# Performance work log

Hardware: AMD Instinct MI355X
Metric: run time of the kernel (lower is better)

The kernel has to match this reference:

```python
import jax, jax.numpy as jnp
import numpy as np

RADIUS_VIEWPOOL = 0.075  # self.view_pool_radius
EPS_BN = 1e-5


def _pconv(x, w, b):
    # 1x1 Conv1d: x (B, Cin, N), w (Cout, Cin), b (Cout,)
    return jnp.einsum('oc,bcn->bon', w, x) + b[None, :, None]


def _bn(x, p):
    # eval-mode BatchNorm1d; p rows: gamma, beta, running_mean, running_var
    g, b, m, v = p[0], p[1], p[2], p[3]
    inv = g * jax.lax.rsqrt(v + EPS_BN)
    return (x - m[None, :, None]) * inv[None, :, None] + b[None, :, None]


def setup_inputs() -> dict:
    key = jax.random.key(0)
    it = iter(jax.random.split(key, 80))
    Np, Nr = 16384, 8192
    inp = {}
    inp['pcd_xyz'] = jax.random.uniform(next(it), (1, Np, 3), jnp.float32)
    inp['rgb_xyz'] = jax.random.uniform(next(it), (1, Nr, 3), jnp.float32)
    inp['pcd_features'] = jax.random.normal(next(it), (1, 32, Np), jnp.float32)
    inp['rgb_features'] = jax.random.normal(next(it), (1, 128, Nr), jnp.float32)

    def conv(name, o, c):
        s = 1.0 / np.sqrt(c)
        inp[name + '_w'] = jax.random.uniform(next(it), (o, c), jnp.float32, -s, s)
        inp[name + '_b'] = jax.random.uniform(next(it), (o,), jnp.float32, -s, s)

    def bn(name, c):
        g = 1.0 + 0.1 * jax.random.normal(next(it), (c,), jnp.float32)
        b = 0.1 * jax.random.normal(next(it), (c,), jnp.float32)
        m = 0.1 * jax.random.normal(next(it), (c,), jnp.float32)
        v = jax.random.uniform(next(it), (c,), jnp.float32, 0.5, 1.5)
        inp[name] = jnp.stack([g, b, m, v])

    conv('cc1', 384, 384); bn('cc_bn', 384); conv('cc2', 128, 384)
    conv('co1', 256, 256); bn('co_bn', 256); conv('co2', 128, 256)
    conv('dh1', 160, 160); bn('dh1_bn', 160)
    conv('dh2', 160, 160); bn('dh2_bn', 160)
    conv('dh3', 128, 160)
    conv('sh1', 128, 128); bn('sh_bn', 128)
    conv('sh2', 1, 128)
    return inp


def _forward(pcd_xyz, rgb_xyz, pcd_features, rgb_features,
             cc1_w, cc1_b, cc_bn, cc2_w, cc2_b,
             co1_w, co1_b, co_bn, co2_w, co2_b,
             dh1_w, dh1_b, dh1_bn, dh2_w, dh2_b, dh2_bn, dh3_w, dh3_b,
             sh1_w, sh1_b, sh_bn, sh2_w, sh2_b):
    Np = pcd_xyz.shape[1]
    Nr = rgb_xyz.shape[1]
    C_rgb = rgb_features.shape[1]

    # ---- three_nn: 3 nearest rgb points for each pcd point ----
    d2 = jnp.sum((pcd_xyz[0, :, None, :] - rgb_xyz[0, None, :, :]) ** 2, axis=-1)  # (Np, Nr)
    neg_d2, idx = jax.lax.top_k(-d2, 3)                     # (Np, 3)
    dist = jnp.sqrt(jnp.maximum(-neg_d2, 0.0))
    # idx[dist > radius] = -1 in torch -> indexes shadow (zero) row appended at end
    neighbor = jnp.where(dist > RADIUS_VIEWPOOL, Nr, idx)   # (Np, 3)

    rgb_f = jnp.concatenate([rgb_features[0].T,
                             jnp.zeros((1, C_rgb), rgb_features.dtype)], axis=0)  # (Nr+1, 128)
    nf = rgb_f[neighbor]                                    # (Np, 3, 128) gather
    max_features = nf.max(axis=1)                           # (Np, 128)

    # fuception fusion: conv over concatenated neighbor features, then fuse with max
    x_cat = nf.reshape(Np, 3 * C_rgb).T[None]               # (1, 384, Np)
    h = jax.nn.relu(_bn(_pconv(x_cat, cc1_w, cc1_b), cc_bn))
    concat_out = _pconv(h, cc2_w, cc2_b)                    # (1, 128, Np)
    x2 = jnp.concatenate([concat_out, max_features.T[None]], axis=1)  # (1, 256, Np)
    h = jax.nn.relu(_bn(_pconv(x2, co1_w, co1_b), co_bn))
    attach = _pconv(h, co2_w, co2_b)                        # (1, 128, Np)

    # fuse pcd + assigned rgb features -> direct feature header (160 = 128+32)
    full = jnp.concatenate([pcd_features, attach], axis=1)  # (1, 160, Np)
    h = jax.nn.relu(_bn(_pconv(full, dh1_w, dh1_b), dh1_bn))
    h = jax.nn.relu(_bn(_pconv(h, dh2_w, dh2_b), dh2_bn))
    fp = _pconv(h, dh3_w, dh3_b)                            # (1, 128, Np)

    # score header: conv-bn-relu-conv-sigmoid
    s = jax.nn.relu(_bn(_pconv(fp, sh1_w, sh1_b), sh_bn))
    vote_scores = jax.nn.sigmoid(_pconv(s, sh2_w, sh2_b))[0, 0]  # (Np,)

    # L2-normalized vote features (N, 128)
    vf = fp[0].T
    vf = vf / jnp.maximum(jnp.linalg.norm(vf, axis=1, keepdims=True), 1e-12)
    return pcd_xyz[0], vote_scores, vf


def reference(pcd_xyz, rgb_xyz, pcd_features, rgb_features,
              cc1_w, cc1_b, cc_bn, cc2_w, cc2_b,
              co1_w, co1_b, co_bn, co2_w, co2_b,
              dh1_w, dh1_b, dh1_bn, dh2_w, dh2_b, dh2_bn, dh3_w, dh3_b,
              sh1_w, sh1_b, sh_bn, sh2_w, sh2_b):
    return _forward(pcd_xyz, rgb_xyz, pcd_features, rgb_features,
                    cc1_w, cc1_b, cc_bn, cc2_w, cc2_b,
                    co1_w, co1_b, co_bn, co2_w, co2_b,
                    dh1_w, dh1_b, dh1_bn, dh2_w, dh2_b, dh2_bn, dh3_w, dh3_b,
                    sh1_w, sh1_b, sh_bn, sh2_w, sh2_b)
```

## Files before the change

kernel.cpp:

```cpp
#include <hip/hip_runtime.h>
#include <math.h>

#define NP 16384
#define NR 8192
#define GRID 13
#define NCELL (GRID * GRID * GRID)
#define CAP 28

typedef __attribute__((ext_vector_type(8))) short short8;
typedef __attribute__((ext_vector_type(4))) float f32x4;

__device__ inline unsigned short f2b(float f) {
  unsigned int x = __float_as_uint(f);
  return (unsigned short)((x + 0x7FFFu + ((x >> 16) & 1u)) >> 16);
}
__device__ inline float blo(unsigned int u) { return __uint_as_float(u << 16); }
__device__ inline float bhi(unsigned int u) { return __uint_as_float(u & 0xffff0000u); }

__global__ __launch_bounds__(256) void k_pre(const float* __restrict__ rf,
                                             const float* __restrict__ rxyz,
                                             const float* __restrict__ pf,
                                             const float* __restrict__ s0, const float* __restrict__ s1,
                                             const float* __restrict__ s2, const float* __restrict__ s3,
                                             const float* __restrict__ s4, const float* __restrict__ s5,
                                             const float* __restrict__ s6, const float* __restrict__ s7,
                                             unsigned short* __restrict__ rgbTb,
                                             float4* __restrict__ rxyz4,
                                             unsigned short* __restrict__ fullp,
                                             unsigned short* __restrict__ dst,
                                             int* __restrict__ cellCnt) {
  __shared__ float tile[128][65];
  int b = blockIdx.x, t = threadIdx.x;
  if (b < 128) {
    int r0 = b * 64;
    for (int e = 0; e < 32; ++e) {
      int idx = t + e * 256;
      int c = idx >> 6, rl = idx & 63;
      tile[c][rl] = rf[c * NR + r0 + rl];
    }
    __syncthreads();
    for (int e = 0; e < 32; ++e) {
      int idx = t + e * 256;
      int rl = idx >> 7, c = idx & 127;
      rgbTb[(size_t)(r0 + rl) * 128 + c] = f2b(tile[c][rl]);
    }
    if (b == 0 && t < 128) rgbTb[(size_t)NR * 128 + t] = 0;
    if ((t >> 6) == 0) {
      int i = r0 + (t & 63);
      float x = rxyz[i * 3], y = rxyz[i * 3 + 1], z = rxyz[i * 3 + 2];
      rxyz4[i] = make_float4(x, y, z, 0.f);
    }
  } else if (b < 384) {
    int n0 = (b - 128) * 64;
    for (int e = 0; e < 8; ++e) {
      int idx = t + e * 256;
      int c = idx >> 6, nl = idx & 63;
      tile[c][nl] = pf[c * NP + n0 + nl];
    }
    __syncthreads();
    for (int e = 0; e < 8; ++e) {
      int idx = t + e * 256;
      int nl = idx >> 5, c = idx & 31;
      fullp[(size_t)(n0 + nl) * 32 + c] = f2b(tile[c][nl]);
    }
  } else if (b < 960) {
    const int groups[8] = {18432, 6144, 8192, 4096, 3200, 3200, 2560, 2048};
    const int Cs[8]     = {384, 384, 256, 256, 160, 160, 160, 128};
    const int offs[8]   = {0, 147456, 196608, 262144, 294912, 320512, 346112, 366592};
    const float* srcs[8] = {s0, s1, s2, s3, s4, s5, s6, s7};
    int j = b - 384;
    int m = j / 72, bx = j % 72;
    int gidx = bx * 256 + t;
    if (gidx >= groups[m]) return;
    int C = Cs[m], NC = C >> 5;
    int ot = gidx / (NC * 64);
    int rem = gidx - ot * (NC * 64);
    int k = rem >> 6, lane = rem & 63;
    int q = lane >> 4, l15 = lane & 15;
    const float* sp = srcs[m] + (size_t)(ot * 16 + l15) * C + k * 32 + q * 8;
    float4 a = *(const float4*)sp, c4 = *(const float4*)(sp + 4);
    uint4 o;
    o.x = f2b(a.x) | ((unsigned int)f2b(a.y) << 16);
    o.y = f2b(a.z) | ((unsigned int)f2b(a.w) << 16);
    o.z = f2b(c4.x) | ((unsigned int)f2b(c4.y) << 16);
    o.w = f2b(c4.z) | ((unsigned int)f2b(c4.w) << 16);
    *(uint4*)(dst + offs[m] + (size_t)gidx * 8) = o;
  } else {
    int idx = (b - 960) * 256 + t;
    if (idx < NCELL) cellCnt[idx] = 0;
  }
}

__global__ __launch_bounds__(64) void k_build(const float4* __restrict__ rxyz4,
                                              int* __restrict__ cellCnt,
                                              float4* __restrict__ cellTab) {
  int i = blockIdx.x * 64 + threadIdx.x;
  float4 r = rxyz4[i];
  int cx = (int)(r.x * 13.f); cx = cx < 0 ? 0 : (cx > 12 ? 12 : cx);
  int cy = (int)(r.y * 13.f); cy = cy < 0 ? 0 : (cy > 12 ? 12 : cy);
  int cz = (int)(r.z * 13.f); cz = cz < 0 ? 0 : (cz > 12 ? 12 : cz);
  int cell = (cz * 13 + cy) * 13 + cx;
  int slot = atomicAdd(&cellCnt[cell], 1);
  if (slot < CAP) cellTab[(size_t)cell * CAP + slot] = make_float4(r.x, r.y, r.z, __int_as_float(i));
}

template <int C, int O, int COFF, bool BN, bool RELU>
__device__ __forceinline__ void mlp_layer(const unsigned short* __restrict__ W,
                                          const float* __restrict__ bias,
                                          const float* __restrict__ bnp,
                                          const unsigned short* Xs,
                                          unsigned short* Ys,
                                          int wo, int q, int l15, int lane) {
  constexpr int NC = C / 32;
  constexpr int NT = O / 16;
  constexpr int MT = (NT + 7) / 8;
  f32x4 acc[MT][2];
  short8 afb[2][MT];
  const unsigned short* wp[MT];
#pragma unroll
  for (int i = 0; i < MT; ++i) {
    acc[i][0] = (f32x4){0.f, 0.f, 0.f, 0.f};
    acc[i][1] = (f32x4){0.f, 0.f, 0.f, 0.f};
    int ot = wo + i * 8;
    wp[i] = W + ((size_t)(((ot < NT) ? ot : 0) * NC) * 64 + lane) * 8;
  }
#pragma unroll
  for (int k = 0; k < 2 && k < NC; ++k)
#pragma unroll
    for (int i = 0; i < MT; ++i)
      if (wo + i * 8 < NT) afb[k][i] = *(const short8*)(wp[i] + (size_t)k * 512);
  short8 bf0 = *(const short8*)&Xs[l15 * 392 + q * 8];
  short8 bf1 = *(const short8*)&Xs[(16 + l15) * 392 + q * 8];
#pragma unroll
  for (int k = 0; k < NC; ++k) {
    short8 nbf0 = bf0, nbf1 = bf1;
    if (k + 1 < NC) {
      nbf0 = *(const short8*)&Xs[l15 * 392 + (k + 1) * 32 + q * 8];
      nbf1 = *(const short8*)&Xs[(16 + l15) * 392 + (k + 1) * 32 + q * 8];
    }
    int slot = k & 1;
#pragma unroll
    for (int i = 0; i < MT; ++i) {
      if (wo + i * 8 < NT) {
        acc[i][0] = __builtin_amdgcn_mfma_f32_16x16x32_bf16(afb[slot][i], bf0, acc[i][0], 0, 0, 0);
        acc[i][1] = __builtin_amdgcn_mfma_f32_16x16x32_bf16(afb[slot][i], bf1, acc[i][1], 0, 0, 0);
      }
    }
    if (k + 2 < NC) {
#pragma unroll
      for (int i = 0; i < MT; ++i)
        if (wo + i * 8 < NT) afb[slot][i] = *(const short8*)(wp[i] + (size_t)(k + 2) * 512);
    }
    bf0 = nbf0; bf1 = nbf1;
  }
#pragma unroll
  for (int i = 0; i < MT; ++i) {
    int ot = wo + i * 8;
    if (ot >= NT) continue;
    int o4 = ot * 16 + q * 4;
    f32x4 bb = *(const f32x4*)(bias + o4);
    f32x4 sc, sh;
    if (BN) {
      f32x4 g  = *(const f32x4*)(bnp + o4);
      f32x4 be = *(const f32x4*)(bnp + O + o4);
      f32x4 mm = *(const f32x4*)(bnp + 2 * O + o4);
      f32x4 vv = *(const f32x4*)(bnp + 3 * O + o4);
#pragma unroll
      for (int r = 0; r < 4; ++r) {
        float inv = g[r] * rsqrtf(vv[r] + 1e-5f);
        sc[r] = inv; sh[r] = (bb[r] - mm[r]) * inv + be[r];
      }
    } else {
      sc = (f32x4){1.f, 1.f, 1.f, 1.f}; sh = bb;
    }
#pragma unroll
    for (int rt = 0; rt < 2; ++rt) {
      ushort4 u;
#pragma unroll
      for (int r = 0; r < 4; ++r) {
        float x = acc[i][rt][r] * sc[r] + sh[r];
        if (RELU) x = fmaxf(x, 0.f);
        ((unsigned short*)&u)[r] = f2b(x);
      }
      *(ushort4*)&Ys[(rt * 16 + l15) * 392 + COFF + ot * 16 + q * 4] = u;
    }
  }
}

__global__ __launch_bounds__(512) void k_mlp(
    const unsigned short* __restrict__ rgbTb,
    const float* __restrict__ pxyz,
    const int* __restrict__ cellCnt,
    const float4* __restrict__ cellTab,
    const unsigned short* __restrict__ fullp,
    const unsigned short* __restrict__ wcc1, const unsigned short* __restrict__ wcc2,
    const unsigned short* __restrict__ wco1, const unsigned short* __restrict__ wco2,
    const unsigned short* __restrict__ wdh1, const unsigned short* __restrict__ wdh2,
    const unsigned short* __restrict__ wdh3, const unsigned short* __restrict__ wsh1,
    const float* __restrict__ cc1_b, const float* __restrict__ cc_bn,
    const float* __restrict__ cc2_b,
    const float* __restrict__ co1_b, const float* __restrict__ co_bn,
    const float* __restrict__ co2_b,
    const float* __restrict__ dh1_b, const float* __restrict__ dh1_bn,
    const float* __restrict__ dh2_b, const float* __restrict__ dh2_bn,
    const float* __restrict__ dh3_b,
    const float* __restrict__ sh1_b, const float* __restrict__ sh_bn,
    const float* __restrict__ sh2_w, const float* __restrict__ sh2_b,
    float* __restrict__ out) {
  __shared__ unsigned short Ab[32 * 392];
  __shared__ unsigned short Bb[32 * 392];
  __shared__ int nbrS[32][3];
  int t = threadIdx.x, lane = t & 63, w = t >> 6;
  int wo = w & 7;
  int q = lane >> 4, l15 = lane & 15;
  int n0 = blockIdx.x * 32;
  {
    int n = n0 + w * 4 + q;
    float px = pxyz[n * 3], py = pxyz[n * 3 + 1], pz = pxyz[n * 3 + 2];
    int cx = (int)(px * 13.f); cx = cx < 0 ? 0 : (cx > 12 ? 12 : cx);
    int cy = (int)(py * 13.f); cy = cy < 0 ? 0 : (cy > 12 ? 12 : cy);
    int cz = (int)(pz * 13.f); cz = cz < 0 ? 0 : (cz > 12 ? 12 : cz);
    const float R2L = 0.005626125f;
    const unsigned long long SENT = ((unsigned long long)__float_as_uint(R2L) << 32);
    unsigned long long k0 = SENT, k1 = SENT, k2 = SENT;
    for (int ci = l15; ci < 27; ci += 16) {
      int dz = ci / 9 - 1, dyc = (ci / 3) % 3 - 1, dxc = ci % 3 - 1;
      int zz = cz + dz, yy = cy + dyc, xx = cx + dxc;
      if ((unsigned)zz <= 12u && (unsigned)yy <= 12u && (unsigned)xx <= 12u) {
        int c = (zz * 13 + yy) * 13 + xx;
        int m = cellCnt[c]; m = m < CAP ? m : CAP;
        const float4* tp = cellTab + (size_t)c * CAP;
        for (int k = 0; k < m; ++k) {
          float4 qq = tp[k];
          float dxx = qq.x - px, dyy = qq.y - py, dzz = qq.z - pz;
          float d2 = fmaf(dxx, dxx, fmaf(dyy, dyy, dzz * dzz));
          unsigned long long key =
              ((unsigned long long)__float_as_uint(d2) << 32) | (unsigned int)__float_as_int(qq.w);
          if (key < k2) {
            if (key < k1) {
              k2 = k1;
              if (key < k0) { k1 = k0; k0 = key; }
              else          { k1 = key; }
            } else k2 = key;
          }
        }
      }
    }
    int pos = 0;
    unsigned long long res[3];
#pragma unroll
    for (int r = 0; r < 3; ++r) {
      unsigned long long cur = (pos == 0) ? k0 : (pos == 1) ? k1 : (pos == 2) ? k2 : ~0ull;
      unsigned long long m = cur;
#pragma unroll
      for (int o = 1; o <= 8; o <<= 1) {
        unsigned long long other = __shfl_xor(m, o);
        m = other < m ? other : m;
      }
      res[r] = m;
      if (cur == m) ++pos;
    }
    if (l15 == 0) {
      const float R2 = 0.075f * 0.075f;
      float d0 = __uint_as_float((unsigned int)(res[0] >> 32));
      float d1 = __uint_as_float((unsigned int)(res[1] >> 32));
      float d2v = __uint_as_float((unsigned int)(res[2] >> 32));
      nbrS[w * 4 + q][0] = (d0 > R2) ? NR : (int)(res[0] & 0xffffffffu);
      nbrS[w * 4 + q][1] = (d1 > R2) ? NR : (int)(res[1] & 0xffffffffu);
      nbrS[w * 4 + q][2] = (d2v > R2) ? NR : (int)(res[2] & 0xffffffffu);
    }
  }
  __syncthreads();
  unsigned int mreg[4];
#pragma unroll
  for (int pj = 0; pj < 4; ++pj) {
    int r = w * 4 + pj;
    unsigned int j0 = (unsigned int)nbrS[r][0]; j0 = j0 > NR ? NR : j0;
    unsigned int j1 = (unsigned int)nbrS[r][1]; j1 = j1 > NR ? NR : j1;
    unsigned int j2 = (unsigned int)nbrS[r][2]; j2 = j2 > NR ? NR : j2;
    unsigned int a = ((const unsigned int*)(rgbTb + (size_t)j0 * 128))[lane];
    unsigned int b = ((const unsigned int*)(rgbTb + (size_t)j1 * 128))[lane];
    unsigned int c = ((const unsigned int*)(rgbTb + (size_t)j2 * 128))[lane];
    unsigned int* xr = (unsigned int*)&Ab[r * 392];
    xr[lane] = a; xr[64 + lane] = b; xr[128 + lane] = c;
    float ml = fmaxf(blo(a), fmaxf(blo(b), blo(c)));
    float mh = fmaxf(bhi(a), fmaxf(bhi(b), bhi(c)));
    mreg[pj] = (__float_as_uint(mh) & 0xffff0000u) | (__float_as_uint(ml) >> 16);
  }
  __syncthreads();
  mlp_layer<384, 384, 0, true,  true >(wcc1, cc1_b, cc_bn, Ab, Bb, wo, q, l15, lane);
  __syncthreads();
#pragma unroll
  for (int pj = 0; pj < 4; ++pj)
    ((unsigned int*)&Ab[(w * 4 + pj) * 392])[64 + lane] = mreg[pj];
  mlp_layer<384, 128, 0, false, false>(wcc2, cc2_b, nullptr, Bb, Ab, wo, q, l15, lane);
  __syncthreads();
  mlp_layer<256, 256, 0, true,  true >(wco1, co1_b, co_bn, Ab, Bb, wo, q, l15, lane);
  __syncthreads();
  mlp_layer<256, 128, 32, false, false>(wco2, co2_b, nullptr, Bb, Ab, wo, q, l15, lane);
  for (int idx = t; idx < 128; idx += 512) {
    int row = idx >> 2, c8 = idx & 3;
    *(uint4*)&Ab[row * 392 + c8 * 8] = *(const uint4*)(fullp + (size_t)(n0 + row) * 32 + c8 * 8);
  }
  __syncthreads();
  mlp_layer<160, 160, 0, true,  true >(wdh1, dh1_b, dh1_bn, Ab, Bb, wo, q, l15, lane);
  __syncthreads();
  mlp_layer<160, 160, 0, true,  true >(wdh2, dh2_b, dh2_bn, Bb, Ab, wo, q, l15, lane);
  __syncthreads();
  mlp_layer<160, 128, 0, false, false>(wdh3, dh3_b, nullptr, Ab, Bb, wo, q, l15, lane);
  __syncthreads();
  mlp_layer<128, 128, 0, true,  true >(wsh1, sh1_b, sh_bn, Bb, Ab, wo, q, l15, lane);
  __syncthreads();
  int col8 = (lane & 15) * 8;
  float4 w0 = *(const float4*)(sh2_w + col8);
  float4 wA = *(const float4*)(sh2_w + col8 + 4);
  float bvv = sh2_b[0];
  int row = w * 4 + (lane >> 4);
  uint4 raw = *(const uint4*)&Ab[row * 392 + col8];
  float acc = blo(raw.x) * w0.x + bhi(raw.x) * w0.y + blo(raw.y) * w0.z + bhi(raw.y) * w0.w +
              blo(raw.z) * wA.x + bhi(raw.z) * wA.y + blo(raw.w) * wA.z + bhi(raw.w) * wA.w;
  acc += __shfl_xor(acc, 1); acc += __shfl_xor(acc, 2);
  acc += __shfl_xor(acc, 4); acc += __shfl_xor(acc, 8);
  if ((lane & 15) == 0) out[49152 + n0 + row] = 1.f / (1.f + expf(-(acc + bvv)));
  uint4 rf = *(const uint4*)&Bb[row * 392 + col8];
  float v[8] = {blo(rf.x), bhi(rf.x), blo(rf.y), bhi(rf.y),
                blo(rf.z), bhi(rf.z), blo(rf.w), bhi(rf.w)};
  float s = 0.f;
#pragma unroll
  for (int i = 0; i < 8; ++i) s = fmaf(v[i], v[i], s);
  s += __shfl_xor(s, 1); s += __shfl_xor(s, 2);
  s += __shfl_xor(s, 4); s += __shfl_xor(s, 8);
  float inv = 1.f / fmaxf(sqrtf(s), 1e-12f);
  float* op = out + 65536 + (size_t)(n0 + row) * 128 + col8;
  *(float4*)op = make_float4(v[0] * inv, v[1] * inv, v[2] * inv, v[3] * inv);
  *(float4*)(op + 4) = make_float4(v[4] * inv, v[5] * inv, v[6] * inv, v[7] * inv);
  for (int i = t; i < 96; i += 512) out[n0 * 3 + i] = pxyz[n0 * 3 + i];
}

extern "C" void kernel_launch(void* const* d_in, const int* in_sizes, int n_in,
                              void* d_out, int out_size, void* d_ws, size_t ws_size,
                              hipStream_t stream) {
  const float* pcd_xyz = (const float*)d_in[0];
  const float* rgb_xyz = (const float*)d_in[1];
  const float* pcd_f   = (const float*)d_in[2];
  const float* rgb_f   = (const float*)d_in[3];
  const float* cc1_w = (const float*)d_in[4];  const float* cc1_b = (const float*)d_in[5];
  const float* cc_bn = (const float*)d_in[6];
  const float* cc2_w = (const float*)d_in[7];  const float* cc2_b = (const float*)d_in[8];
  const float* co1_w = (const float*)d_in[9];  const float* co1_b = (const float*)d_in[10];
  const float* co_bn = (const float*)d_in[11];
  const float* co2_w = (const float*)d_in[12]; const float* co2_b = (const float*)d_in[13];
  const float* dh1_w = (const float*)d_in[14]; const float* dh1_b = (const float*)d_in[15];
  const float* dh1_bn = (const float*)d_in[16];
  const float* dh2_w = (const float*)d_in[17]; const float* dh2_b = (const float*)d_in[18];
  const float* dh2_bn = (const float*)d_in[19];
  const float* dh3_w = (const float*)d_in[20]; const float* dh3_b = (const float*)d_in[21];
  const float* sh1_w = (const float*)d_in[22]; const float* sh1_b = (const float*)d_in[23];
  const float* sh_bn = (const float*)d_in[24];
  const float* sh2_w = (const float*)d_in[25]; const float* sh2_b = (const float*)d_in[26];

  char* ws = (char*)d_ws;
  float* out = (float*)d_out;

  unsigned short* wb    = (unsigned short*)(ws);
  unsigned short* rgbTb = (unsigned short*)(ws + 0x100000);
  float4* rxyz4         = (float4*)(ws + 0x320000);
  int*    cellCnt       = (int*)(ws + 0x480000);
  float4* cellTab       = (float4*)(ws + 0x490000);
  unsigned short* fullp = (unsigned short*)(ws + 0xA00000);

  unsigned short* wb_cc1 = wb;
  unsigned short* wb_cc2 = wb + 147456;
  unsigned short* wb_co1 = wb + 196608;
  unsigned short* wb_co2 = wb + 262144;
  unsigned short* wb_dh1 = wb + 294912;
  unsigned short* wb_dh2 = wb + 320512;
  unsigned short* wb_dh3 = wb + 346112;
  unsigned short* wb_sh1 = wb + 366592;

  k_pre<<<969, 256, 0, stream>>>(rgb_f, rgb_xyz, pcd_f,
                                 cc1_w, cc2_w, co1_w, co2_w, dh1_w, dh2_w, dh3_w, sh1_w,
                                 rgbTb, rxyz4, fullp, wb, cellCnt);
  k_build<<<128, 64, 0, stream>>>(rxyz4, cellCnt, cellTab);
  k_mlp<<<512, 512, 0, stream>>>(rgbTb, pcd_xyz, cellCnt, cellTab, fullp,
                                 wb_cc1, wb_cc2, wb_co1, wb_co2,
                                 wb_dh1, wb_dh2, wb_dh3, wb_sh1,
                                 cc1_b, cc_bn, cc2_b, co1_b, co_bn, co2_b,
                                 dh1_b, dh1_bn, dh2_b, dh2_bn, dh3_b,
                                 sh1_b, sh_bn, sh2_w, sh2_b,
                                 out);
}
```

Measured before the change: 152.9 us.

## Double points per block in fused MLP kernel to reuse weight fragments

Measured after the change: 158.5 us. 3.6% more time.

```diff
diff --git a/kernel.cpp b/kernel.cpp
--- a/kernel.cpp
+++ b/kernel.cpp
@@ -114,13 +114,13 @@
   constexpr int NC = C / 32;
   constexpr int NT = O / 16;
   constexpr int MT = (NT + 7) / 8;
-  f32x4 acc[MT][2];
+  f32x4 acc[MT][4];
   short8 afb[2][MT];
   const unsigned short* wp[MT];
 #pragma unroll
   for (int i = 0; i < MT; ++i) {
-    acc[i][0] = (f32x4){0.f, 0.f, 0.f, 0.f};
-    acc[i][1] = (f32x4){0.f, 0.f, 0.f, 0.f};
+#pragma unroll
+    for (int rt = 0; rt < 4; ++rt) acc[i][rt] = (f32x4){0.f, 0.f, 0.f, 0.f};
     int ot = wo + i * 8;
     wp[i] = W + ((size_t)(((ot < NT) ? ot : 0) * NC) * 64 + lane) * 8;
   }
@@ -129,21 +129,25 @@
 #pragma unroll
     for (int i = 0; i < MT; ++i)
       if (wo + i * 8 < NT) afb[k][i] = *(const short8*)(wp[i] + (size_t)k * 512);
-  short8 bf0 = *(const short8*)&Xs[l15 * 392 + q * 8];
-  short8 bf1 = *(const short8*)&Xs[(16 + l15) * 392 + q * 8];
+  short8 bf[4];
+#pragma unroll
+  for (int rt = 0; rt < 4; ++rt) bf[rt] = *(const short8*)&Xs[(rt * 16 + l15) * 392 + q * 8];
 #pragma unroll
   for (int k = 0; k < NC; ++k) {
-    short8 nbf0 = bf0, nbf1 = bf1;
-    if (k + 1 < NC) {
-      nbf0 = *(const short8*)&Xs[l15 * 392 + (k + 1) * 32 + q * 8];
-      nbf1 = *(const short8*)&Xs[(16 + l15) * 392 + (k + 1) * 32 + q * 8];
+    short8 nbf[4];
+#pragma unroll
+    for (int rt = 0; rt < 4; ++rt) {
+      nbf[rt] = bf[rt];
+      if (k + 1 < NC)
+        nbf[rt] = *(const short8*)&Xs[(rt * 16 + l15) * 392 + (k + 1) * 32 + q * 8];
     }
     int slot = k & 1;
 #pragma unroll
     for (int i = 0; i < MT; ++i) {
       if (wo + i * 8 < NT) {
-        acc[i][0] = __builtin_amdgcn_mfma_f32_16x16x32_bf16(afb[slot][i], bf0, acc[i][0], 0, 0, 0);
-        acc[i][1] = __builtin_amdgcn_mfma_f32_16x16x32_bf16(afb[slot][i], bf1, acc[i][1], 0, 0, 0);
+#pragma unroll
+        for (int rt = 0; rt < 4; ++rt)
+          acc[i][rt] = __builtin_amdgcn_mfma_f32_16x16x32_bf16(afb[slot][i], bf[rt], acc[i][rt], 0, 0, 0);
       }
     }
     if (k + 2 < NC) {
@@ -151,7 +155,8 @@
       for (int i = 0; i < MT; ++i)
         if (wo + i * 8 < NT) afb[slot][i] = *(const short8*)(wp[i] + (size_t)(k + 2) * 512);
     }
-    bf0 = nbf0; bf1 = nbf1;
+#pragma unroll
+    for (int rt = 0; rt < 4; ++rt) bf[rt] = nbf[rt];
   }
 #pragma unroll
   for (int i = 0; i < MT; ++i) {
@@ -174,7 +179,7 @@
       sc = (f32x4){1.f, 1.f, 1.f, 1.f}; sh = bb;
     }
 #pragma unroll
-    for (int rt = 0; rt < 2; ++rt) {
+    for (int rt = 0; rt < 4; ++rt) {
       ushort4 u;
 #pragma unroll
       for (int r = 0; r < 4; ++r) {
@@ -207,15 +212,16 @@
     const float* __restrict__ sh1_b, const float* __restrict__ sh_bn,
     const float* __restrict__ sh2_w, const float* __restrict__ sh2_b,
     float* __restrict__ out) {
-  __shared__ unsigned short Ab[32 * 392];
-  __shared__ unsigned short Bb[32 * 392];
-  __shared__ int nbrS[32][3];
+  __shared__ unsigned short Ab[64 * 392];
+  __shared__ unsigned short Bb[64 * 392];
+  __shared__ int nbrS[64][3];
   int t = threadIdx.x, lane = t & 63, w = t >> 6;
-  int wo = w & 7;
+  int wo = w;
   int q = lane >> 4, l15 = lane & 15;
-  int n0 = blockIdx.x * 32;
+  int n0 = blockIdx.x * 64;
   {
-    int n = n0 + w * 4 + q;
+    int nq = t >> 3, l8 = t & 7;
+    int n = n0 + nq;
     float px = pxyz[n * 3], py = pxyz[n * 3 + 1], pz = pxyz[n * 3 + 2];
     int cx = (int)(px * 13.f); cx = cx < 0 ? 0 : (cx > 12 ? 12 : cx);
     int cy = (int)(py * 13.f); cy = cy < 0 ? 0 : (cy > 12 ? 12 : cy);
@@ -223,7 +229,7 @@
     const float R2L = 0.005626125f;
     const unsigned long long SENT = ((unsigned long long)__float_as_uint(R2L) << 32);
     unsigned long long k0 = SENT, k1 = SENT, k2 = SENT;
-    for (int ci = l15; ci < 27; ci += 16) {
+    for (int ci = l8; ci < 27; ci += 8) {
       int dz = ci / 9 - 1, dyc = (ci / 3) % 3 - 1, dxc = ci % 3 - 1;
       int zz = cz + dz, yy = cy + dyc, xx = cx + dxc;
       if ((unsigned)zz <= 12u && (unsigned)yy <= 12u && (unsigned)xx <= 12u) {
@@ -253,28 +259,28 @@
       unsigned long long cur = (pos == 0) ? k0 : (pos == 1) ? k1 : (pos == 2) ? k2 : ~0ull;
       unsigned long long m = cur;
 #pragma unroll
-      for (int o = 1; o <= 8; o <<= 1) {
+      for (int o = 1; o <= 4; o <<= 1) {
         unsigned long long other = __shfl_xor(m, o);
         m = other < m ? other : m;
       }
       res[r] = m;
       if (cur == m) ++pos;
     }
-    if (l15 == 0) {
+    if (l8 == 0) {
       const float R2 = 0.075f * 0.075f;
       float d0 = __uint_as_float((unsigned int)(res[0] >> 32));
       float d1 = __uint_as_float((unsigned int)(res[1] >> 32));
       float d2v = __uint_as_float((unsigned int)(res[2] >> 32));
-      nbrS[w * 4 + q][0] = (d0 > R2) ? NR : (int)(res[0] & 0xffffffffu);
-      nbrS[w * 4 + q][1] = (d1 > R2) ? NR : (int)(res[1] & 0xffffffffu);
-      nbrS[w * 4 + q][2] = (d2v > R2) ? NR : (int)(res[2] & 0xffffffffu);
-    }
-  }
-  __syncthreads();
-  unsigned int mreg[4];
-#pragma unroll
-  for (int pj = 0; pj < 4; ++pj) {
-    int r = w * 4 + pj;
+      nbrS[nq][0] = (d0 > R2) ? NR : (int)(res[0] & 0xffffffffu);
+      nbrS[nq][1] = (d1 > R2) ? NR : (int)(res[1] & 0xffffffffu);
+      nbrS[nq][2] = (d2v > R2) ? NR : (int)(res[2] & 0xffffffffu);
+    }
+  }
+  __syncthreads();
+  unsigned int mreg[8];
+#pragma unroll
+  for (int pj = 0; pj < 8; ++pj) {
+    int r = w * 8 + pj;
     unsigned int j0 = (unsigned int)nbrS[r][0]; j0 = j0 > NR ? NR : j0;
     unsigned int j1 = (unsigned int)nbrS[r][1]; j1 = j1 > NR ? NR : j1;
     unsigned int j2 = (unsigned int)nbrS[r][2]; j2 = j2 > NR ? NR : j2;
@@ -291,14 +297,14 @@
   mlp_layer<384, 384, 0, true,  true >(wcc1, cc1_b, cc_bn, Ab, Bb, wo, q, l15, lane);
   __syncthreads();
 #pragma unroll
-  for (int pj = 0; pj < 4; ++pj)
-    ((unsigned int*)&Ab[(w * 4 + pj) * 392])[64 + lane] = mreg[pj];
+  for (int pj = 0; pj < 8; ++pj)
+    ((unsigned int*)&Ab[(w * 8 + pj) * 392])[64 + lane] = mreg[pj];
   mlp_layer<384, 128, 0, false, false>(wcc2, cc2_b, nullptr, Bb, Ab, wo, q, l15, lane);
   __syncthreads();
   mlp_layer<256, 256, 0, true,  true >(wco1, co1_b, co_bn, Ab, Bb, wo, q, l15, lane);
   __syncthreads();
   mlp_layer<256, 128, 32, false, false>(wco2, co2_b, nullptr, Bb, Ab, wo, q, l15, lane);
-  for (int idx = t; idx < 128; idx += 512) {
+  for (int idx = t; idx < 256; idx += 512) {
     int row = idx >> 2, c8 = idx & 3;
     *(uint4*)&Ab[row * 392 + c8 * 8] = *(const uint4*)(fullp + (size_t)(n0 + row) * 32 + c8 * 8);
   }
@@ -315,26 +321,29 @@
   float4 w0 = *(const float4*)(sh2_w + col8);
   float4 wA = *(const float4*)(sh2_w + col8 + 4);
   float bvv = sh2_b[0];
-  int row = w * 4 + (lane >> 4);
-  uint4 raw = *(const uint4*)&Ab[row * 392 + col8];
-  float acc = blo(raw.x) * w0.x + bhi(raw.x) * w0.y + blo(raw.y) * w0.z + bhi(raw.y) * w0.w +
-              blo(raw.z) * wA.x + bhi(raw.z) * wA.y + blo(raw.w) * wA.z + bhi(raw.w) * wA.w;
-  acc += __shfl_xor(acc, 1); acc += __shfl_xor(acc, 2);
-  acc += __shfl_xor(acc, 4); acc += __shfl_xor(acc, 8);
-  if ((lane & 15) == 0) out[49152 + n0 + row] = 1.f / (1.f + expf(-(acc + bvv)));
-  uint4 rf = *(const uint4*)&Bb[row * 392 + col8];
-  float v[8] = {blo(rf.x), bhi(rf.x), blo(rf.y), bhi(rf.y),
-                blo(rf.z), bhi(rf.z), blo(rf.w), bhi(rf.w)};
-  float s = 0.f;
-#pragma unroll
-  for (int i = 0; i < 8; ++i) s = fmaf(v[i], v[i], s);
-  s += __shfl_xor(s, 1); s += __shfl_xor(s, 2);
-  s += __shfl_xor(s, 4); s += __shfl_xor(s, 8);
-  float inv = 1.f / fmaxf(sqrtf(s), 1e-12f);
-  float* op = out + 65536 + (size_t)(n0 + row) * 128 + col8;
-  *(float4*)op = make_float4(v[0] * inv, v[1] * inv, v[2] * inv, v[3] * inv);
-  *(float4*)(op + 4) = make_float4(v[4] * inv, v[5] * inv, v[6] * inv, v[7] * inv);
-  for (int i = t; i < 96; i += 512) out[n0 * 3 + i] = pxyz[n0 * 3 + i];
+#pragma unroll
+  for (int pr = 0; pr < 2; ++pr) {
+    int row = w * 8 + pr * 4 + (lane >> 4);
+    uint4 raw = *(const uint4*)&Ab[row * 392 + col8];
+    float acc = blo(raw.x) * w0.x + bhi(raw.x) * w0.y + blo(raw.y) * w0.z + bhi(raw.y) * w0.w +
+                blo(raw.z) * wA.x + bhi(raw.z) * wA.y + blo(raw.w) * wA.z + bhi(raw.w) * wA.w;
+    acc += __shfl_xor(acc, 1); acc += __shfl_xor(acc, 2);
+    acc += __shfl_xor(acc, 4); acc += __shfl_xor(acc, 8);
+    if ((lane & 15) == 0) out[49152 + n0 + row] = 1.f / (1.f + expf(-(acc + bvv)));
+    uint4 rf = *(const uint4*)&Bb[row * 392 + col8];
+    float v[8] = {blo(rf.x), bhi(rf.x), blo(rf.y), bhi(rf.y),
+                  blo(rf.z), bhi(rf.z), blo(rf.w), bhi(rf.w)};
+    float s = 0.f;
+#pragma unroll
+    for (int i = 0; i < 8; ++i) s = fmaf(v[i], v[i], s);
+    s += __shfl_xor(s, 1); s += __shfl_xor(s, 2);
+    s += __shfl_xor(s, 4); s += __shfl_xor(s, 8);
+    float inv = 1.f / fmaxf(sqrtf(s), 1e-12f);
+    float* op = out + 65536 + (size_t)(n0 + row) * 128 + col8;
+    *(float4*)op = make_float4(v[0] * inv, v[1] * inv, v[2] * inv, v[3] * inv);
+    *(float4*)(op + 4) = make_float4(v[4] * inv, v[5] * inv, v[6] * inv, v[7] * inv);
+  }
+  for (int i = t; i < 192; i += 512) out[n0 * 3 + i] = pxyz[n0 * 3 + i];
 }
 
 extern "C" void kernel_launch(void* const* d_in, const int* in_sizes, int n_in,
@@ -382,7 +391,7 @@
                                  cc1_w, cc2_w, co1_w, co2_w, dh1_w, dh2_w, dh3_w, sh1_w,
                                  rgbTb, rxyz4, fullp, wb, cellCnt);
   k_build<<<128, 64, 0, stream>>>(rxyz4, cellCnt, cellTab);
-  k_mlp<<<512, 512, 0, stream>>>(rgbTb, pcd_xyz, cellCnt, cellTab, fullp,
+  k_mlp<<<256, 512, 0, stream>>>(rgbTb, pcd_xyz, cellCnt, cellTab, fullp,
                                  wb_cc1, wb_cc2, wb_co1, wb_co2,
                                  wb_dh1, wb_dh2, wb_dh3, wb_sh1,
                                  cc1_b, cc_bn, cc2_b, co1_b, co_bn, co2_b,
```

## Prefetch next layer weights before barriers and pass neighbors via shuffles

Applied to the files above, without the earlier changes.

Result: no change. 154.5 us (+1.0%).

```diff
diff --git a/kernel.cpp b/kernel.cpp
--- a/kernel.cpp
+++ b/kernel.cpp
@@ -104,8 +104,34 @@
   if (slot < CAP) cellTab[(size_t)cell * CAP + slot] = make_float4(r.x, r.y, r.z, __int_as_float(i));
 }
 
+template <int C, int O>
+struct WPre {
+  static constexpr int NT = O / 16;
+  static constexpr int MT = (NT + 7) / 8;
+  const unsigned short* wp[MT];
+  short8 afb[3][MT];
+};
+
+template <int C, int O>
+__device__ __forceinline__ void wpre(const unsigned short* __restrict__ W, int wo, int lane,
+                                     WPre<C, O>& P) {
+  constexpr int NC = C / 32;
+  constexpr int NT = O / 16;
+  constexpr int MT = (NT + 7) / 8;
+#pragma unroll
+  for (int i = 0; i < MT; ++i) {
+    int ot = wo + i * 8;
+    P.wp[i] = W + ((size_t)(((ot < NT) ? ot : 0) * NC) * 64 + lane) * 8;
+  }
+#pragma unroll
+  for (int k = 0; k < 3 && k < NC; ++k)
+#pragma unroll
+    for (int i = 0; i < MT; ++i)
+      if (wo + i * 8 < NT) P.afb[k][i] = *(const short8*)(P.wp[i] + (size_t)k * 512);
+}
+
 template <int C, int O, int COFF, bool BN, bool RELU>
-__device__ __forceinline__ void mlp_layer(const unsigned short* __restrict__ W,
+__device__ __forceinline__ void mlp_layer(WPre<C, O>& P,
                                           const float* __restrict__ bias,
                                           const float* __restrict__ bnp,
                                           const unsigned short* Xs,
@@ -115,20 +141,11 @@
   constexpr int NT = O / 16;
   constexpr int MT = (NT + 7) / 8;
   f32x4 acc[MT][2];
-  short8 afb[2][MT];
-  const unsigned short* wp[MT];
 #pragma unroll
   for (int i = 0; i < MT; ++i) {
     acc[i][0] = (f32x4){0.f, 0.f, 0.f, 0.f};
     acc[i][1] = (f32x4){0.f, 0.f, 0.f, 0.f};
-    int ot = wo + i * 8;
-    wp[i] = W + ((size_t)(((ot < NT) ? ot : 0) * NC) * 64 + lane) * 8;
-  }
-#pragma unroll
-  for (int k = 0; k < 2 && k < NC; ++k)
-#pragma unroll
-    for (int i = 0; i < MT; ++i)
-      if (wo + i * 8 < NT) afb[k][i] = *(const short8*)(wp[i] + (size_t)k * 512);
+  }
   short8 bf0 = *(const short8*)&Xs[l15 * 392 + q * 8];
   short8 bf1 = *(const short8*)&Xs[(16 + l15) * 392 + q * 8];
 #pragma unroll
@@ -138,18 +155,18 @@
       nbf0 = *(const short8*)&Xs[l15 * 392 + (k + 1) * 32 + q * 8];
       nbf1 = *(const short8*)&Xs[(16 + l15) * 392 + (k + 1) * 32 + q * 8];
     }
-    int slot = k & 1;
+    int slot = k % 3;
 #pragma unroll
     for (int i = 0; i < MT; ++i) {
       if (wo + i * 8 < NT) {
-        acc[i][0] = __builtin_amdgcn_mfma_f32_16x16x32_bf16(afb[slot][i], bf0, acc[i][0], 0, 0, 0);
-        acc[i][1] = __builtin_amdgcn_mfma_f32_16x16x32_bf16(afb[slot][i], bf1, acc[i][1], 0, 0, 0);
+        acc[i][0] = __builtin_amdgcn_mfma_f32_16x16x32_bf16(P.afb[slot][i], bf0, acc[i][0], 0, 0, 0);
+        acc[i][1] = __builtin_amdgcn_mfma_f32_16x16x32_bf16(P.afb[slot][i], bf1, acc[i][1], 0, 0, 0);
       }
     }
-    if (k + 2 < NC) {
+    if (k + 3 < NC) {
 #pragma unroll
       for (int i = 0; i < MT; ++i)
-        if (wo + i * 8 < NT) afb[slot][i] = *(const short8*)(wp[i] + (size_t)(k + 2) * 512);
+        if (wo + i * 8 < NT) P.afb[slot][i] = *(const short8*)(P.wp[i] + (size_t)(k + 3) * 512);
     }
     bf0 = nbf0; bf1 = nbf1;
   }
@@ -187,7 +204,7 @@
   }
 }
 
-__global__ __launch_bounds__(512) void k_mlp(
+__global__ __launch_bounds__(512, 4) void k_mlp(
     const unsigned short* __restrict__ rgbTb,
     const float* __restrict__ pxyz,
     const int* __restrict__ cellCnt,
@@ -209,11 +226,12 @@
     float* __restrict__ out) {
   __shared__ unsigned short Ab[32 * 392];
   __shared__ unsigned short Bb[32 * 392];
-  __shared__ int nbrS[32][3];
   int t = threadIdx.x, lane = t & 63, w = t >> 6;
   int wo = w & 7;
   int q = lane >> 4, l15 = lane & 15;
   int n0 = blockIdx.x * 32;
+  WPre<384, 384> Pcc1; wpre<384, 384>(wcc1, wo, lane, Pcc1);
+  int j0, j1, j2;
   {
     int n = n0 + w * 4 + q;
     float px = pxyz[n * 3], py = pxyz[n * 3 + 1], pz = pxyz[n * 3 + 2];
@@ -260,27 +278,24 @@
       res[r] = m;
       if (cur == m) ++pos;
     }
-    if (l15 == 0) {
-      const float R2 = 0.075f * 0.075f;
-      float d0 = __uint_as_float((unsigned int)(res[0] >> 32));
-      float d1 = __uint_as_float((unsigned int)(res[1] >> 32));
-      float d2v = __uint_as_float((unsigned int)(res[2] >> 32));
-      nbrS[w * 4 + q][0] = (d0 > R2) ? NR : (int)(res[0] & 0xffffffffu);
-      nbrS[w * 4 + q][1] = (d1 > R2) ? NR : (int)(res[1] & 0xffffffffu);
-      nbrS[w * 4 + q][2] = (d2v > R2) ? NR : (int)(res[2] & 0xffffffffu);
-    }
-  }
-  __syncthreads();
+    const float R2 = 0.075f * 0.075f;
+    float d0 = __uint_as_float((unsigned int)(res[0] >> 32));
+    float d1 = __uint_as_float((unsigned int)(res[1] >> 32));
+    float d2v = __uint_as_float((unsigned int)(res[2] >> 32));
+    j0 = (d0 > R2) ? NR : (int)(res[0] & 0xffffffffu);
+    j1 = (d1 > R2) ? NR : (int)(res[1] & 0xffffffffu);
+    j2 = (d2v > R2) ? NR : (int)(res[2] & 0xffffffffu);
+  }
   unsigned int mreg[4];
 #pragma unroll
   for (int pj = 0; pj < 4; ++pj) {
     int r = w * 4 + pj;
-    unsigned int j0 = (unsigned int)nbrS[r][0]; j0 = j0 > NR ? NR : j0;
-    unsigned int j1 = (unsigned int)nbrS[r][1]; j1 = j1 > NR ? NR : j1;
-    unsigned int j2 = (unsigned int)nbrS[r][2]; j2 = j2 > NR ? NR : j2;
-    unsigned int a = ((const unsigned int*)(rgbTb + (size_t)j0 * 128))[lane];
-    unsigned int b = ((const unsigned int*)(rgbTb + (size_t)j1 * 128))[lane];
-    unsigned int c = ((const unsigned int*)(rgbTb + (size_t)j2 * 128))[lane];
+    unsigned int g0 = (unsigned int)__shfl(j0, pj * 16); g0 = g0 > NR ? NR : g0;
+    unsigned int g1 = (unsigned int)__shfl(j1, pj * 16); g1 = g1 > NR ? NR : g1;
+    unsigned int g2 = (unsigned int)__shfl(j2, pj * 16); g2 = g2 > NR ? NR : g2;
+    unsigned int a = ((const unsigned int*)(rgbTb + (size_t)g0 * 128))[lane];
+    unsigned int b = ((const unsigned int*)(rgbTb + (size_t)g1 * 128))[lane];
+    unsigned int c = ((const unsigned int*)(rgbTb + (size_t)g2 * 128))[lane];
     unsigned int* xr = (unsigned int*)&Ab[r * 392];
     xr[lane] = a; xr[64 + lane] = b; xr[128 + lane] = c;
     float ml = fmaxf(blo(a), fmaxf(blo(b), blo(c)));
@@ -288,28 +303,35 @@
     mreg[pj] = (__float_as_uint(mh) & 0xffff0000u) | (__float_as_uint(ml) >> 16);
   }
   __syncthreads();
-  mlp_layer<384, 384, 0, true,  true >(wcc1, cc1_b, cc_bn, Ab, Bb, wo, q, l15, lane);
+  mlp_layer<384, 384, 0, true,  true >(Pcc1, cc1_b, cc_bn, Ab, Bb, wo, q, l15, lane);
+  WPre<384, 128> Pcc2; wpre<384, 128>(wcc2, wo, lane, Pcc2);
   __syncthreads();
 #pragma unroll
   for (int pj = 0; pj < 4; ++pj)
     ((unsigned int*)&Ab[(w * 4 + pj) * 392])[64 + lane] = mreg[pj];
-  mlp_layer<384, 128, 0, false, false>(wcc2, cc2_b, nullptr, Bb, Ab, wo, q, l15, lane);
-  __syncthreads();
-  mlp_layer<256, 256, 0, true,  true >(wco1, co1_b, co_bn, Ab, Bb, wo, q, l15, lane);
-  __syncthreads();
-  mlp_layer<256, 128, 32, false, false>(wco2, co2_b, nullptr, Bb, Ab, wo, q, l15, lane);
+  mlp_layer<384, 128, 0, false, false>(Pcc2, cc2_b, nullptr, Bb, Ab, wo, q, l15, lane);
+  WPre<256, 256> Pco1; wpre<256, 256>(wco1, wo, lane, Pco1);
+  __syncthreads();
+  mlp_layer<256, 256, 0, true,  true >(Pco1, co1_b, co_bn, Ab, Bb, wo, q, l15, lane);
+  WPre<256, 128> Pco2; wpre<256, 128>(wco2, wo, lane, Pco2);
+  __syncthreads();
+  mlp_layer<256, 128, 32, false, false>(Pco2, co2_b, nullptr, Bb, Ab, wo, q, l15, lane);
   for (int idx = t; idx < 128; idx += 512) {
     int row = idx >> 2, c8 = idx & 3;
     *(uint4*)&Ab[row * 392 + c8 * 8] = *(const uint4*)(fullp + (size_t)(n0 + row) * 32 + c8 * 8);
   }
-  __syncthreads();
-  mlp_layer<160, 160, 0, true,  true >(wdh1, dh1_b, dh1_bn, Ab, Bb, wo, q, l15, lane);
-  __syncthreads();
-  mlp_layer<160, 160, 0, true,  true >(wdh2, dh2_b, dh2_bn, Bb, Ab, wo, q, l15, lane);
-  __syncthreads();
-  mlp_layer<160, 128, 0, false, false>(wdh3, dh3_b, nullptr, Ab, Bb, wo, q, l15, lane);
-  __syncthreads();
-  mlp_layer<128, 128, 0, true,  true >(wsh1, sh1_b, sh_bn, Bb, Ab, wo, q, l15, lane);
+  WPre<160, 160> Pdh1; wpre<160, 160>(wdh1, wo, lane, Pdh1);
+  __syncthreads();
+  mlp_layer<160, 160, 0, true,  true >(Pdh1, dh1_b, dh1_bn, Ab, Bb, wo, q, l15, lane);
+  WPre<160, 160> Pdh2; wpre<160, 160>(wdh2, wo, lane, Pdh2);
+  __syncthreads();
+  mlp_layer<160, 160, 0, true,  true >(Pdh2, dh2_b, dh2_bn, Bb, Ab, wo, q, l15, lane);
+  WPre<160, 128> Pdh3; wpre<160, 128>(wdh3, wo, lane, Pdh3);
+  __syncthreads();
+  mlp_layer<160, 128, 0, false, false>(Pdh3, dh3_b, nullptr, Ab, Bb, wo, q, l15, lane);
+  WPre<128, 128> Psh1; wpre<128, 128>(wsh1, wo, lane, Psh1);
+  __syncthreads();
+  mlp_layer<128, 128, 0, true,  true >(Psh1, sh1_b, sh_bn, Bb, Ab, wo, q, l15, lane);
   __syncthreads();
   int col8 = (lane & 15) * 8;
   float4 w0 = *(const float4*)(sh2_w + col8);
```

## Halve points per block in fused MLP kernel and compute neighbors per lane-half

Applied to the files above, without the earlier changes.

New measurement: 188.6 us. 23.3% more time.

```diff
diff --git a/kernel.cpp b/kernel.cpp
--- a/kernel.cpp
+++ b/kernel.cpp
@@ -114,13 +114,12 @@
   constexpr int NC = C / 32;
   constexpr int NT = O / 16;
   constexpr int MT = (NT + 7) / 8;
-  f32x4 acc[MT][2];
+  f32x4 acc[MT];
   short8 afb[2][MT];
   const unsigned short* wp[MT];
 #pragma unroll
   for (int i = 0; i < MT; ++i) {
-    acc[i][0] = (f32x4){0.f, 0.f, 0.f, 0.f};
-    acc[i][1] = (f32x4){0.f, 0.f, 0.f, 0.f};
+    acc[i] = (f32x4){0.f, 0.f, 0.f, 0.f};
     int ot = wo + i * 8;
     wp[i] = W + ((size_t)(((ot < NT) ? ot : 0) * NC) * 64 + lane) * 8;
   }
@@ -130,28 +129,23 @@
     for (int i = 0; i < MT; ++i)
       if (wo + i * 8 < NT) afb[k][i] = *(const short8*)(wp[i] + (size_t)k * 512);
   short8 bf0 = *(const short8*)&Xs[l15 * 392 + q * 8];
-  short8 bf1 = *(const short8*)&Xs[(16 + l15) * 392 + q * 8];
 #pragma unroll
   for (int k = 0; k < NC; ++k) {
-    short8 nbf0 = bf0, nbf1 = bf1;
-    if (k + 1 < NC) {
+    short8 nbf0 = bf0;
+    if (k + 1 < NC)
       nbf0 = *(const short8*)&Xs[l15 * 392 + (k + 1) * 32 + q * 8];
-      nbf1 = *(const short8*)&Xs[(16 + l15) * 392 + (k + 1) * 32 + q * 8];
-    }
     int slot = k & 1;
 #pragma unroll
     for (int i = 0; i < MT; ++i) {
-      if (wo + i * 8 < NT) {
-        acc[i][0] = __builtin_amdgcn_mfma_f32_16x16x32_bf16(afb[slot][i], bf0, acc[i][0], 0, 0, 0);
-        acc[i][1] = __builtin_amdgcn_mfma_f32_16x16x32_bf16(afb[slot][i], bf1, acc[i][1], 0, 0, 0);
-      }
+      if (wo + i * 8 < NT)
+        acc[i] = __builtin_amdgcn_mfma_f32_16x16x32_bf16(afb[slot][i], bf0, acc[i], 0, 0, 0);
     }
     if (k + 2 < NC) {
 #pragma unroll
       for (int i = 0; i < MT; ++i)
         if (wo + i * 8 < NT) afb[slot][i] = *(const short8*)(wp[i] + (size_t)(k + 2) * 512);
     }
-    bf0 = nbf0; bf1 = nbf1;
+    bf0 = nbf0;
   }
 #pragma unroll
   for (int i = 0; i < MT; ++i) {
@@ -173,21 +167,18 @@
     } else {
       sc = (f32x4){1.f, 1.f, 1.f, 1.f}; sh = bb;
     }
-#pragma unroll
-    for (int rt = 0; rt < 2; ++rt) {
-      ushort4 u;
-#pragma unroll
-      for (int r = 0; r < 4; ++r) {
-        float x = acc[i][rt][r] * sc[r] + sh[r];
-        if (RELU) x = fmaxf(x, 0.f);
-        ((unsigned short*)&u)[r] = f2b(x);
-      }
-      *(ushort4*)&Ys[(rt * 16 + l15) * 392 + COFF + ot * 16 + q * 4] = u;
-    }
-  }
-}
-
-__global__ __launch_bounds__(512) void k_mlp(
+    ushort4 u;
+#pragma unroll
+    for (int r = 0; r < 4; ++r) {
+      float x = acc[i][r] * sc[r] + sh[r];
+      if (RELU) x = fmaxf(x, 0.f);
+      ((unsigned short*)&u)[r] = f2b(x);
+    }
+    *(ushort4*)&Ys[l15 * 392 + COFF + ot * 16 + q * 4] = u;
+  }
+}
+
+__global__ __launch_bounds__(512, 8) void k_mlp(
     const unsigned short* __restrict__ rgbTb,
     const float* __restrict__ pxyz,
     const int* __restrict__ cellCnt,
@@ -207,15 +198,15 @@
     const float* __restrict__ sh1_b, const float* __restrict__ sh_bn,
     const float* __restrict__ sh2_w, const float* __restrict__ sh2_b,
     float* __restrict__ out) {
-  __shared__ unsigned short Ab[32 * 392];
-  __shared__ unsigned short Bb[32 * 392];
-  __shared__ int nbrS[32][3];
+  __shared__ unsigned short Ab[16 * 392];
+  __shared__ unsigned short Bb[16 * 392];
   int t = threadIdx.x, lane = t & 63, w = t >> 6;
-  int wo = w & 7;
+  int wo = w;
   int q = lane >> 4, l15 = lane & 15;
-  int n0 = blockIdx.x * 32;
+  int n0 = blockIdx.x * 16;
+  int j0, j1, j2;
   {
-    int n = n0 + w * 4 + q;
+    int n = n0 + (t >> 5), l32 = t & 31;
     float px = pxyz[n * 3], py = pxyz[n * 3 + 1], pz = pxyz[n * 3 + 2];
     int cx = (int)(px * 13.f); cx = cx < 0 ? 0 : (cx > 12 ? 12 : cx);
     int cy = (int)(py * 13.f); cy = cy < 0 ? 0 : (cy > 12 ? 12 : cy);
@@ -223,8 +214,8 @@
     const float R2L = 0.005626125f;
     const unsigned long long SENT = ((unsigned long long)__float_as_uint(R2L) << 32);
     unsigned long long k0 = SENT, k1 = SENT, k2 = SENT;
-    for (int ci = l15; ci < 27; ci += 16) {
-      int dz = ci / 9 - 1, dyc = (ci / 3) % 3 - 1, dxc = ci % 3 - 1;
+    if (l32 < 27) {
+      int dz = l32 / 9 - 1, dyc = (l32 / 3) % 3 - 1, dxc = l32 % 3 - 1;
       int zz = cz + dz, yy = cy + dyc, xx = cx + dxc;
       if ((unsigned)zz <= 12u && (unsigned)yy <= 12u && (unsigned)xx <= 12u) {
         int c = (zz * 13 + yy) * 13 + xx;
@@ -253,34 +244,31 @@
       unsigned long long cur = (pos == 0) ? k0 : (pos == 1) ? k1 : (pos == 2) ? k2 : ~0ull;
       unsigned long long m = cur;
 #pragma unroll
-      for (int o = 1; o <= 8; o <<= 1) {
+      for (int o = 1; o <= 16; o <<= 1) {
         unsigned long long other = __shfl_xor(m, o);
         m = other < m ? other : m;
       }
       res[r] = m;
       if (cur == m) ++pos;
     }
-    if (l15 == 0) {
-      const float R2 = 0.075f * 0.075f;
-      float d0 = __uint_as_float((unsigned int)(res[0] >> 32));
-      float d1 = __uint_as_float((unsigned int)(res[1] >> 32));
-      float d2v = __uint_as_float((unsigned int)(res[2] >> 32));
-      nbrS[w * 4 + q][0] = (d0 > R2) ? NR : (int)(res[0] & 0xffffffffu);
-      nbrS[w * 4 + q][1] = (d1 > R2) ? NR : (int)(res[1] & 0xffffffffu);
-      nbrS[w * 4 + q][2] = (d2v > R2) ? NR : (int)(res[2] & 0xffffffffu);
-    }
-  }
-  __syncthreads();
-  unsigned int mreg[4];
-#pragma unroll
-  for (int pj = 0; pj < 4; ++pj) {
-    int r = w * 4 + pj;
-    unsigned int j0 = (unsigned int)nbrS[r][0]; j0 = j0 > NR ? NR : j0;
-    unsigned int j1 = (unsigned int)nbrS[r][1]; j1 = j1 > NR ? NR : j1;
-    unsigned int j2 = (unsigned int)nbrS[r][2]; j2 = j2 > NR ? NR : j2;
-    unsigned int a = ((const unsigned int*)(rgbTb + (size_t)j0 * 128))[lane];
-    unsigned int b = ((const unsigned int*)(rgbTb + (size_t)j1 * 128))[lane];
-    unsigned int c = ((const unsigned int*)(rgbTb + (size_t)j2 * 128))[lane];
+    const float R2 = 0.075f * 0.075f;
+    float d0 = __uint_as_float((unsigned int)(res[0] >> 32));
+    float d1 = __uint_as_float((unsigned int)(res[1] >> 32));
+    float d2v = __uint_as_float((unsigned int)(res[2] >> 32));
+    j0 = (d0 > R2) ? NR : (int)(res[0] & 0xffffffffu);
+    j1 = (d1 > R2) ? NR : (int)(res[1] & 0xffffffffu);
+    j2 = (d2v > R2) ? NR : (int)(res[2] & 0xffffffffu);
+  }
+  unsigned int mreg[2];
+#pragma unroll
+  for (int pj = 0; pj < 2; ++pj) {
+    int r = w * 2 + pj;
+    unsigned int g0 = (unsigned int)__shfl(j0, pj * 32); g0 = g0 > NR ? NR : g0;
+    unsigned int g1 = (unsigned int)__shfl(j1, pj * 32); g1 = g1 > NR ? NR : g1;
+    unsigned int g2 = (unsigned int)__shfl(j2, pj * 32); g2 = g2 > NR ? NR : g2;
+    unsigned int a = ((const unsigned int*)(rgbTb + (size_t)g0 * 128))[lane];
+    unsigned int b = ((const unsigned int*)(rgbTb + (size_t)g1 * 128))[lane];
+    unsigned int c = ((const unsigned int*)(rgbTb + (size_t)g2 * 128))[lane];
     unsigned int* xr = (unsigned int*)&Ab[r * 392];
     xr[lane] = a; xr[64 + lane] = b; xr[128 + lane] = c;
     float ml = fmaxf(blo(a), fmaxf(blo(b), blo(c)));
@@ -291,15 +279,15 @@
   mlp_layer<384, 384, 0, true,  true >(wcc1, cc1_b, cc_bn, Ab, Bb, wo, q, l15, lane);
   __syncthreads();
 #pragma unroll
-  for (int pj = 0; pj < 4; ++pj)
-    ((unsigned int*)&Ab[(w * 4 + pj) * 392])[64 + lane] = mreg[pj];
+  for (int pj = 0; pj < 2; ++pj)
+    ((unsigned int*)&Ab[(w * 2 + pj) * 392])[64 + lane] = mreg[pj];
   mlp_layer<384, 128, 0, false, false>(wcc2, cc2_b, nullptr, Bb, Ab, wo, q, l15, lane);
   __syncthreads();
   mlp_layer<256, 256, 0, true,  true >(wco1, co1_b, co_bn, Ab, Bb, wo, q, l15, lane);
   __syncthreads();
   mlp_layer<256, 128, 32, false, false>(wco2, co2_b, nullptr, Bb, Ab, wo, q, l15, lane);
-  for (int idx = t; idx < 128; idx += 512) {
-    int row = idx >> 2, c8 = idx & 3;
+  if (t < 64) {
+    int row = t >> 2, c8 = t & 3;
     *(uint4*)&Ab[row * 392 + c8 * 8] = *(const uint4*)(fullp + (size_t)(n0 + row) * 32 + c8 * 8);
   }
   __syncthreads();
@@ -311,30 +299,33 @@
   __syncthreads();
   mlp_layer<128, 128, 0, true,  true >(wsh1, sh1_b, sh_bn, Bb, Ab, wo, q, l15, lane);
   __syncthreads();
-  int col8 = (lane & 15) * 8;
+  int s = lane & 31;
+  int col8 = (s & 15) * 8;
   float4 w0 = *(const float4*)(sh2_w + col8);
   float4 wA = *(const float4*)(sh2_w + col8 + 4);
   float bvv = sh2_b[0];
-  int row = w * 4 + (lane >> 4);
+  int row = w * 2 + (lane >> 5);
   uint4 raw = *(const uint4*)&Ab[row * 392 + col8];
   float acc = blo(raw.x) * w0.x + bhi(raw.x) * w0.y + blo(raw.y) * w0.z + bhi(raw.y) * w0.w +
               blo(raw.z) * wA.x + bhi(raw.z) * wA.y + blo(raw.w) * wA.z + bhi(raw.w) * wA.w;
   acc += __shfl_xor(acc, 1); acc += __shfl_xor(acc, 2);
   acc += __shfl_xor(acc, 4); acc += __shfl_xor(acc, 8);
-  if ((lane & 15) == 0) out[49152 + n0 + row] = 1.f / (1.f + expf(-(acc + bvv)));
+  if (s == 0) out[49152 + n0 + row] = 1.f / (1.f + expf(-(acc + bvv)));
   uint4 rf = *(const uint4*)&Bb[row * 392 + col8];
   float v[8] = {blo(rf.x), bhi(rf.x), blo(rf.y), bhi(rf.y),
                 blo(rf.z), bhi(rf.z), blo(rf.w), bhi(rf.w)};
-  float s = 0.f;
-#pragma unroll
-  for (int i = 0; i < 8; ++i) s = fmaf(v[i], v[i], s);
-  s += __shfl_xor(s, 1); s += __shfl_xor(s, 2);
-  s += __shfl_xor(s, 4); s += __shfl_xor(s, 8);
-  float inv = 1.f / fmaxf(sqrtf(s), 1e-12f);
-  float* op = out + 65536 + (size_t)(n0 + row) * 128 + col8;
-  *(float4*)op = make_float4(v[0] * inv, v[1] * inv, v[2] * inv, v[3] * inv);
-  *(float4*)(op + 4) = make_float4(v[4] * inv, v[5] * inv, v[6] * inv, v[7] * inv);
-  for (int i = t; i < 96; i += 512) out[n0 * 3 + i] = pxyz[n0 * 3 + i];
+  float ss = 0.f;
+#pragma unroll
+  for (int i = 0; i < 8; ++i) ss = fmaf(v[i], v[i], ss);
+  ss += __shfl_xor(ss, 1); ss += __shfl_xor(ss, 2);
+  ss += __shfl_xor(ss, 4); ss += __shfl_xor(ss, 8);
+  float inv = 1.f / fmaxf(sqrtf(ss), 1e-12f);
+  if (s < 16) {
+    float* op = out + 65536 + (size_t)(n0 + row) * 128 + col8;
+    *(float4*)op = make_float4(v[0] * inv, v[1] * inv, v[2] * inv, v[3] * inv);
+    *(float4*)(op + 4) = make_float4(v[4] * inv, v[5] * inv, v[6] * inv, v[7] * inv);
+  }
+  if (t < 48) out[n0 * 3 + t] = pxyz[n0 * 3 + t];
 }
 
 extern "C" void kernel_launch(void* const* d_in, const int* in_sizes, int n_in,
@@ -382,11 +373,11 @@
                                  cc1_w, cc2_w, co1_w, co2_w, dh1_w, dh2_w, dh3_w, sh1_w,
                                  rgbTb, rxyz4, fullp, wb, cellCnt);
   k_build<<<128, 64, 0, stream>>>(rxyz4, cellCnt, cellTab);
-  k_mlp<<<512, 512, 0, stream>>>(rgbTb, pcd_xyz, cellCnt, cellTab, fullp,
-                                 wb_cc1, wb_cc2, wb_co1, wb_co2,
-                                 wb_dh1, wb_dh2, wb_dh3, wb_sh1,
-                                 cc1_b, cc_bn, cc2_b, co1_b, co_bn, co2_b,
-                                 dh1_b, dh1_bn, dh2_b, dh2_bn, dh3_b,
-                                 sh1_b, sh_bn, sh2_w, sh2_b,
-                                 out);
-}
+  k_mlp<<<1024, 512, 0, stream>>>(rgbTb, pcd_xyz, cellCnt, cellTab, fullp,
+                                  wb_cc1, wb_cc2, wb_co1, wb_co2,
+                                  wb_dh1, wb_dh2, wb_dh3, wb_sh1,
+                                  cc1_b, cc_bn, cc2_b, co1_b, co_bn, co2_b,
+                                  dh1_b, dh1_bn, dh2_b, dh2_bn, dh3_b,
+                                  sh1_b, sh_bn, sh2_w, sh2_b,
+                                  out);
+}
```
